# Kernel tuning notes

Hardware: AMD Instinct MI355X
Metric: run time of the kernel (lower is better)

Reference implementation:

```python
import jax, jax.numpy as jnp
import numpy as np

B, S, E = 256, 128, 1024


def setup_inputs() -> dict:
    key = jax.random.key(0)
    k1, k2, k3, k4, k5 = jax.random.split(key, 5)
    x = jax.random.normal(k1, (B, S, E), dtype=jnp.float32)
    # ragged bags: start in [0,32), length in [1,96] so end <= 128 and bags are non-empty
    starts = jax.random.randint(k2, (B,), 0, 32)
    lengths = jax.random.randint(k3, (B,), 1, 97)
    document_index = jnp.stack([starts, starts + lengths], axis=-1).astype(jnp.int32)  # [B,2]
    scale = 1.0 / np.sqrt(E)
    W = jax.random.normal(k4, (E, E), dtype=jnp.float32) * scale  # relationMatrix.weight
    u = jax.random.normal(k5, (1, E), dtype=jnp.float32) * scale  # relationVector.weight
    return {"x": x, "W": W, "u": u, "document_index": document_index}


def reference(x, W, u, document_index):
    # scores_bs = relationVector(tanh(relationMatrix(x)))  (bias-free linears)
    h = jnp.tanh(jnp.einsum('bse,fe->bsf', x, W))          # [B,S,E]
    scores = jnp.einsum('bse,e->bs', h, u[0])              # [B,S]
    # ragged mask: position s belongs to doc b iff start <= s < end
    idx = jnp.arange(S)[None, :]                            # [1,S]
    mask = (idx >= document_index[:, :1]) & (idx < document_index[:, 1:])  # [B,S]
    attn = jax.nn.softmax(jnp.where(mask, scores, -jnp.inf), axis=-1)      # [B,S]
    attn = jnp.where(mask, attn, 0.0)
    out_concat = jnp.einsum('bs,bse->be', attn, x)          # [B,E]
    # keep_attention in the original is the last bag's softmax weights;
    # here returned padded to length S (zeros outside the bag)
    keep_attention = attn[-1]                               # [S]
    return out_concat, keep_attention
```

## Files before the change

### kernel.cpp

```cpp
#include <hip/hip_runtime.h>
#include <math.h>

#define Bb 256
#define Ss 128
#define Ee 1024
#define BK 64
#define APAD 72
#define NMAX 2048

typedef __bf16 bf16x8 __attribute__((ext_vector_type(8)));
typedef float f32x4 __attribute__((ext_vector_type(4)));

typedef __attribute__((address_space(3))) unsigned int lds_u32;
typedef __attribute__((address_space(1))) unsigned int glb_u32;

static __device__ __forceinline__ unsigned short f2bf(float f) {
    unsigned int u = __float_as_uint(f);
    u += 0x7FFFu + ((u >> 16) & 1u);
    return (unsigned short)(u >> 16);
}
static __device__ __forceinline__ float bf2f(unsigned short h) {
    return __uint_as_float((unsigned int)h << 16);
}

__global__ void conv_all(const float* __restrict__ x,
                         const float* __restrict__ W,
                         const int* __restrict__ doc,
                         unsigned short* __restrict__ xb,
                         unsigned short* __restrict__ Wb,
                         int* __restrict__ list) {
    const int st = blockIdx.x, by = blockIdx.y, tid = threadIdx.x;
    if (by == Bb + 128) {
        if (st != 0) return;
        __shared__ int sc[256];
        const int b = tid;
        const int start = doc[2 * b], end = doc[2 * b + 1];
        const int s0 = start >> 4;
        const int ns = ((end + 15) >> 4) - s0;
        sc[b] = ns;
        __syncthreads();
        for (int d = 1; d < 256; d <<= 1) {
            int v = sc[b];
            int add = (b >= d) ? sc[b - d] : 0;
            __syncthreads();
            sc[b] = v + add;
            __syncthreads();
        }
        const int total = sc[255];
        const int off = sc[b] - ns;
        for (int i = 0; i < ns; ++i)
            list[off + i] = b * Ss + ((s0 + i) << 4);
        for (int i = total + b; i < NMAX; i += 256)
            list[i] = -1;
        return;
    }
    if (by >= Bb) {
        int i = ((((by - Bb) << 3) | st) << 8) | tid;
        float4 v = reinterpret_cast<const float4*>(W)[i];
        ushort4 o;
        o.x = f2bf(v.x); o.y = f2bf(v.y); o.z = f2bf(v.z); o.w = f2bf(v.w);
        reinterpret_cast<ushort4*>(Wb)[i] = o;
        return;
    }
    const int b = by;
    const int start = doc[2 * b], end = doc[2 * b + 1];
    const int strip0 = start >> 4;
    const int ns = ((end + 15) >> 4) - strip0;
    if (st < strip0 || st >= strip0 + ns) return;
    const size_t base = ((size_t)b * Ss + (st << 4)) * Ee;
    #pragma unroll
    for (int r = 0; r < 16; ++r) {
        size_t idx = base + (size_t)r * Ee + (tid << 2);
        float4 v = *reinterpret_cast<const float4*>(x + idx);
        ushort4 o;
        o.x = f2bf(v.x); o.y = f2bf(v.y); o.z = f2bf(v.z); o.w = f2bf(v.w);
        *reinterpret_cast<ushort4*>(xb + idx) = o;
    }
}

__global__ void convW_kernel(const float* __restrict__ W, unsigned short* __restrict__ Wb) {
    int i = blockIdx.x * blockDim.x + threadIdx.x;
    float4 v = reinterpret_cast<const float4*>(W)[i];
    ushort4 o;
    o.x = f2bf(v.x); o.y = f2bf(v.y); o.z = f2bf(v.z); o.w = f2bf(v.w);
    reinterpret_cast<ushort4*>(Wb)[i] = o;
}

__launch_bounds__(256, 4)
__global__ void scores_gemm_xb(const unsigned short* __restrict__ xb,
                               const unsigned short* __restrict__ Wb,
                               const float* __restrict__ u,
                               const int* __restrict__ list,
                               float* __restrict__ part) {
    __shared__ __align__(16) unsigned short As[64 * BK];
    __shared__ __align__(16) unsigned short Bs[256 * BK];

    const int mb = blockIdx.x;
    const int fg = blockIdx.y;

    int e0 = list[mb << 2];
    if (e0 < 0) return;
    int e[4];
    bool val[4];
    e[0] = e0; val[0] = true;
    #pragma unroll
    for (int j = 1; j < 4; ++j) {
        int v = list[(mb << 2) | j];
        val[j] = v >= 0;
        e[j] = val[j] ? v : e0;
    }

    const int tid  = threadIdx.x;
    const int wave = tid >> 6;
    const int lane = tid & 63;
    const int quad = lane >> 4;
    const int l16  = lane & 15;

    const unsigned short* wbase = Wb + (size_t)(fg * 256) * Ee;

    f32x4 acc[4][4];
    #pragma unroll
    for (int i = 0; i < 4; ++i)
        #pragma unroll
        for (int j = 0; j < 4; ++j) acc[i][j] = (f32x4){0.f, 0.f, 0.f, 0.f};

    for (int t = 0; t < 16; ++t) {
        const int k0 = t << 6;
        #pragma unroll
        for (int r = 0; r < 2; ++r) {
            int chunk = (r << 8) | tid;
            int arow = chunk >> 3;
            int c8 = (chunk & 7) ^ (arow & 7);
            __builtin_amdgcn_global_load_lds(
                (const glb_u32*)(xb + ((size_t)e[arow >> 4] + (arow & 15)) * Ee + k0 + (c8 << 3)),
                (lds_u32*)&As[chunk << 3], 16, 0, 0);
        }
        #pragma unroll
        for (int r = 0; r < 8; ++r) {
            int chunk = (r << 8) | tid;
            int brow = chunk >> 3;
            int c8 = (chunk & 7) ^ (brow & 7);
            __builtin_amdgcn_global_load_lds(
                (const glb_u32*)(wbase + (size_t)brow * Ee + k0 + (c8 << 3)),
                (lds_u32*)&Bs[chunk << 3], 16, 0, 0);
        }
        __syncthreads();

        #pragma unroll
        for (int kk = 0; kk < BK; kk += 32) {
            const int c8k = (kk >> 3) + quad;
            bf16x8 bf[4];
            #pragma unroll
            for (int j = 0; j < 4; ++j) {
                const int n = wave * 64 + j * 16 + l16;
                bf[j] = *reinterpret_cast<const bf16x8*>(
                    &Bs[((n << 3) | (c8k ^ (n & 7))) << 3]);
            }
            #pragma unroll
            for (int st = 0; st < 4; ++st) {
                const int ar = st * 16 + l16;
                bf16x8 af = *reinterpret_cast<const bf16x8*>(
                    &As[((ar << 3) | (c8k ^ (ar & 7))) << 3]);
                #pragma unroll
                for (int j = 0; j < 4; ++j)
                    acc[st][j] = __builtin_amdgcn_mfma_f32_16x16x32_bf16(af, bf[j], acc[st][j], 0, 0, 0);
            }
        }
        __syncthreads();
    }

    float* s_red = reinterpret_cast<float*>(As);
    float uj[4];
    #pragma unroll
    for (int j = 0; j < 4; ++j)
        uj[j] = u[fg * 256 + wave * 64 + j * 16 + l16];
    #pragma unroll
    for (int st = 0; st < 4; ++st) {
        float p[4];
        #pragma unroll
        for (int r = 0; r < 4; ++r) {
            p[r] = tanhf(acc[st][0][r]) * uj[0] + tanhf(acc[st][1][r]) * uj[1]
                 + tanhf(acc[st][2][r]) * uj[2] + tanhf(acc[st][3][r]) * uj[3];
        }
        #pragma unroll
        for (int off = 8; off >= 1; off >>= 1)
            #pragma unroll
            for (int r = 0; r < 4; ++r)
                p[r] += __shfl_xor(p[r], off, 16);
        if (l16 == 0)
            #pragma unroll
            for (int r = 0; r < 4; ++r)
                s_red[wave * 64 + st * 16 + quad * 4 + r] = p[r];
    }
    __syncthreads();
    if (tid < 64) {
        const int strip = tid >> 4;
        if (val[strip]) {
            float v = s_red[tid] + s_red[64 + tid] + s_red[128 + tid] + s_red[192 + tid];
            part[(((size_t)e[strip] + (tid & 15)) << 2) | fg] = v;
        }
    }
}

__launch_bounds__(256)
__global__ void scores_gemm_fb(const float* __restrict__ x,
                               const unsigned short* __restrict__ Wb,
                               const float* __restrict__ u,
                               const int* __restrict__ doc,
                               float* __restrict__ part) {
    __shared__ __align__(16) unsigned short As[8 * 16 * APAD];
    __shared__ __align__(16) unsigned short Bs[128 * BK];
    __shared__ float s_red[4][128];

    const int b  = blockIdx.x;
    const int ft = blockIdx.y;
    const int start = doc[2 * b], end = doc[2 * b + 1];
    const int strip0 = start >> 4;
    const int ns = ((end + 15) >> 4) - strip0;
    const int row0 = strip0 << 4;

    const int tid  = threadIdx.x;
    const int wave = tid >> 6;
    const int lane = tid & 63;
    const int quad = lane >> 4;
    const int l16  = lane & 15;
    const int arow = tid >> 4;
    const int acol = (tid & 15) << 2;

    const float* xbase = x + ((size_t)b * Ss + row0) * Ee;
    const unsigned short* wbase = Wb + (size_t)ft * 128 * Ee;

    f32x4 acc[8][2];
    #pragma unroll
    for (int i = 0; i < 8; ++i)
        #pragma unroll
        for (int j = 0; j < 2; ++j) acc[i][j] = (f32x4){0.f, 0.f, 0.f, 0.f};

    for (int k0 = 0; k0 < Ee; k0 += BK) {
        #pragma unroll
        for (int r = 0; r < 8; ++r) if (r < ns) {
            int row = (r << 4) | arow;
            float4 v = *reinterpret_cast<const float4*>(xbase + (size_t)row * Ee + k0 + acol);
            ushort4 o; o.x = f2bf(v.x); o.y = f2bf(v.y); o.z = f2bf(v.z); o.w = f2bf(v.w);
            *reinterpret_cast<ushort4*>(&As[row * APAD + acol]) = o;
        }
        #pragma unroll
        for (int r = 0; r < 4; ++r) {
            int chunk = (r << 8) | tid;
            int brow = chunk >> 3;
            int c8 = (chunk & 7) ^ (brow & 7);
            __builtin_amdgcn_global_load_lds(
                (const glb_u32*)(wbase + (size_t)brow * Ee + k0 + (c8 << 3)),
                (lds_u32*)&Bs[chunk << 3], 16, 0, 0);
        }
        __syncthreads();
        #pragma unroll
        for (int kk = 0; kk < BK; kk += 32) {
            const int n0 = wave * 32 + l16;
            const int n1 = n0 + 16;
            const int c8k = (kk >> 3) + quad;
            bf16x8 bf0 = *reinterpret_cast<const bf16x8*>(
                &Bs[((n0 << 3) | (c8k ^ (n0 & 7))) << 3]);
            bf16x8 bf1 = *reinterpret_cast<const bf16x8*>(
                &Bs[((n1 << 3) | (c8k ^ (n1 & 7))) << 3]);
            #pragma unroll
            for (int st = 0; st < 8; ++st) {
                if (st < ns) {
                    bf16x8 af = *reinterpret_cast<const bf16x8*>(
                        &As[(st * 16 + l16) * APAD + kk + quad * 8]);
                    acc[st][0] = __builtin_amdgcn_mfma_f32_16x16x32_bf16(af, bf0, acc[st][0], 0, 0, 0);
                    acc[st][1] = __builtin_amdgcn_mfma_f32_16x16x32_bf16(af, bf1, acc[st][1], 0, 0, 0);
                }
            }
        }
        __syncthreads();
    }

    const float u0 = u[ft * 128 + wave * 32 + l16];
    const float u1 = u[ft * 128 + wave * 32 + 16 + l16];
    #pragma unroll
    for (int st = 0; st < 8; ++st) {
        if (st < ns) {
            float p[4];
            #pragma unroll
            for (int r = 0; r < 4; ++r)
                p[r] = tanhf(acc[st][0][r]) * u0 + tanhf(acc[st][1][r]) * u1;
            #pragma unroll
            for (int off = 8; off >= 1; off >>= 1)
                #pragma unroll
                for (int r = 0; r < 4; ++r)
                    p[r] += __shfl_xor(p[r], off, 16);
            if (l16 == 0)
                #pragma unroll
                for (int r = 0; r < 4; ++r)
                    s_red[wave][st * 16 + quad * 4 + r] = p[r];
        }
    }
    __syncthreads();
    if (tid < (ns << 4)) {
        float v = s_red[0][tid] + s_red[1][tid] + s_red[2][tid] + s_red[3][tid];
        part[((size_t)(b * Ss + row0 + tid) << 3) | ft] = v;
    }
}

__global__ void out_fused(const unsigned short* __restrict__ xb,
                          const float* __restrict__ x,
                          const float* __restrict__ part,
                          const int* __restrict__ doc,
                          float* __restrict__ out,
                          float* __restrict__ keep,
                          int np8) {
    const int h = blockIdx.x, b = blockIdx.y, t = threadIdx.x;
    const int start = doc[2 * b], end = doc[2 * b + 1];
    __shared__ float a_s[Ss];
    __shared__ float red[2];
    __shared__ float4 red4[4][64];

    bool m = false;
    float sc = -INFINITY;
    if (t < Ss) {
        m = (t >= start) && (t < end);
        if (m) {
            const float* pp = part + (size_t)(b * Ss + t) * (np8 ? 8 : 4);
            float4 p0 = *reinterpret_cast<const float4*>(pp);
            sc = (p0.x + p0.y) + (p0.z + p0.w);
            if (np8) {
                float4 p1 = *reinterpret_cast<const float4*>(pp + 4);
                sc += (p1.x + p1.y) + (p1.z + p1.w);
            }
        }
    }
    float v = sc;
    #pragma unroll
    for (int off = 32; off >= 1; off >>= 1)
        v = fmaxf(v, __shfl_xor(v, off, 64));
    if (t < Ss && (t & 63) == 0) red[t >> 6] = v;
    __syncthreads();
    const float mx = fmaxf(red[0], red[1]);
    __syncthreads();
    const float e = m ? __expf(sc - mx) : 0.f;
    v = e;
    #pragma unroll
    for (int off = 32; off >= 1; off >>= 1)
        v += __shfl_xor(v, off, 64);
    if (t < Ss && (t & 63) == 0) red[t >> 6] = v;
    __syncthreads();
    if (t < Ss) a_s[t] = e / (red[0] + red[1]);
    __syncthreads();
    if (h == 0 && b == Bb - 1 && t < Ss) keep[t] = a_s[t];

    const int ssub = t >> 6, tt = t & 63;
    float4 accv = {0.f, 0.f, 0.f, 0.f};
    if (xb) {
        const unsigned short* xr = xb + (size_t)b * Ss * Ee + h * 256 + (tt << 2);
        for (int s = start + ssub; s < end; s += 4) {
            float a = a_s[s];
            ushort4 q = *reinterpret_cast<const ushort4*>(xr + (size_t)s * Ee);
            accv.x += a * bf2f(q.x); accv.y += a * bf2f(q.y);
            accv.z += a * bf2f(q.z); accv.w += a * bf2f(q.w);
        }
    } else {
        const float* xr = x + (size_t)b * Ss * Ee + h * 256 + (tt << 2);
        for (int s = start + ssub; s < end; s += 4) {
            float a = a_s[s];
            float4 q = *reinterpret_cast<const float4*>(xr + (size_t)s * Ee);
            accv.x += a * q.x; accv.y += a * q.y;
            accv.z += a * q.z; accv.w += a * q.w;
        }
    }
    red4[ssub][tt] = accv;
    __syncthreads();
    if (t < 64) {
        float4 r0 = red4[0][t], r1 = red4[1][t], r2 = red4[2][t], r3 = red4[3][t];
        float4 s;
        s.x = (r0.x + r1.x) + (r2.x + r3.x);
        s.y = (r0.y + r1.y) + (r2.y + r3.y);
        s.z = (r0.z + r1.z) + (r2.z + r3.z);
        s.w = (r0.w + r1.w) + (r2.w + r3.w);
        reinterpret_cast<float4*>(out + (size_t)b * Ee + h * 256)[t] = s;
    }
}

extern "C" void kernel_launch(void* const* d_in, const int* in_sizes, int n_in,
                              void* d_out, int out_size, void* d_ws, size_t ws_size,
                              hipStream_t stream) {
    const float* x  = (const float*)d_in[0];
    const float* W  = (const float*)d_in[1];
    const float* u  = (const float*)d_in[2];
    const int* doc  = (const int*)d_in[3];
    float* out = (float*)d_out;

    const size_t szWb   = (size_t)Ee * Ee * 2;
    const size_t szXb   = (size_t)Bb * Ss * Ee * 2;
    const size_t szPart = (size_t)Bb * Ss * 8 * 4;
    const size_t szList = (size_t)NMAX * 4;

    unsigned short* Wb = (unsigned short*)d_ws;
    const bool big_ws = ws_size >= szWb + szXb + szPart + szList;

    if (big_ws) {
        unsigned short* xbuf = (unsigned short*)((char*)d_ws + szWb);
        float* part = (float*)((char*)d_ws + szWb + szXb);
        int* list = (int*)((char*)d_ws + szWb + szXb + szPart);
        conv_all<<<dim3(8, Bb + 129), 256, 0, stream>>>(x, W, doc, xbuf, Wb, list);
        scores_gemm_xb<<<dim3(NMAX / 4, 4), 256, 0, stream>>>(xbuf, Wb, u, list, part);
        out_fused<<<dim3(4, Bb), 256, 0, stream>>>(xbuf, x, part, doc, out, out + (size_t)Bb * Ee, 0);
    } else {
        float* part = (float*)((char*)d_ws + szWb);
        convW_kernel<<<1024, 256, 0, stream>>>(W, Wb);
        scores_gemm_fb<<<dim3(Bb, 8), 256, 0, stream>>>(x, Wb, u, doc, part);
        out_fused<<<dim3(4, Bb), 256, 0, stream>>>(nullptr, x, part, doc, out, out + (size_t)Bb * Ee, 1);
    }
}
```

Measured before the change: 245.6 us.

## Load W fragments directly from global and double-buffer A tiles in LDS

The scores GEMM on the xb path no longer stages the W tile through LDS. Each lane reads its bf16x8 W fragments straight from global memory into registers, and only the x tile is staged, now in two LDS buffers so the next k-slice loads while the current one computes. This cuts LDS footprint and the per-iteration W staging and barrier work. In exchange, W reads are uncoalesced per-lane global loads that depend on cache hits, and the occupancy hint drops from 4 to 3 waves.

```diff
diff --git a/kernel.cpp b/kernel.cpp
--- a/kernel.cpp
+++ b/kernel.cpp
@@ -86,14 +86,14 @@
     reinterpret_cast<ushort4*>(Wb)[i] = o;
 }
 
-__launch_bounds__(256, 4)
+__launch_bounds__(256, 3)
 __global__ void scores_gemm_xb(const unsigned short* __restrict__ xb,
                                const unsigned short* __restrict__ Wb,
                                const float* __restrict__ u,
                                const int* __restrict__ list,
                                float* __restrict__ part) {
-    __shared__ __align__(16) unsigned short As[64 * BK];
-    __shared__ __align__(16) unsigned short Bs[256 * BK];
+    __shared__ __align__(16) unsigned short As[2][64 * BK];
+    __shared__ float s_red[4][64];
 
     const int mb = blockIdx.x;
     const int fg = blockIdx.y;
@@ -116,7 +116,7 @@
     const int quad = lane >> 4;
     const int l16  = lane & 15;
 
-    const unsigned short* wbase = Wb + (size_t)(fg * 256) * Ee;
+    const unsigned short* wrow = Wb + (size_t)(fg * 256 + wave * 64 + l16) * Ee + quad * 8;
 
     f32x4 acc[4][4];
     #pragma unroll
@@ -124,8 +124,7 @@
         #pragma unroll
         for (int j = 0; j < 4; ++j) acc[i][j] = (f32x4){0.f, 0.f, 0.f, 0.f};
 
-    for (int t = 0; t < 16; ++t) {
-        const int k0 = t << 6;
+    auto stageA = [&](int buf, int k0) {
         #pragma unroll
         for (int r = 0; r < 2; ++r) {
             int chunk = (r << 8) | tid;
@@ -133,34 +132,30 @@
             int c8 = (chunk & 7) ^ (arow & 7);
             __builtin_amdgcn_global_load_lds(
                 (const glb_u32*)(xb + ((size_t)e[arow >> 4] + (arow & 15)) * Ee + k0 + (c8 << 3)),
-                (lds_u32*)&As[chunk << 3], 16, 0, 0);
-        }
-        #pragma unroll
-        for (int r = 0; r < 8; ++r) {
-            int chunk = (r << 8) | tid;
-            int brow = chunk >> 3;
-            int c8 = (chunk & 7) ^ (brow & 7);
-            __builtin_amdgcn_global_load_lds(
-                (const glb_u32*)(wbase + (size_t)brow * Ee + k0 + (c8 << 3)),
-                (lds_u32*)&Bs[chunk << 3], 16, 0, 0);
-        }
-        __syncthreads();
+                (lds_u32*)&As[buf][chunk << 3], 16, 0, 0);
+        }
+    };
+
+    stageA(0, 0);
+    __syncthreads();
+
+    for (int t = 0; t < 16; ++t) {
+        const int k0 = t << 6;
+        const int cb = t & 1, nb = cb ^ 1;
+        if (t < 15) stageA(nb, k0 + 64);
 
         #pragma unroll
         for (int kk = 0; kk < BK; kk += 32) {
+            bf16x8 bf[4];
+            #pragma unroll
+            for (int j = 0; j < 4; ++j)
+                bf[j] = *reinterpret_cast<const bf16x8*>(wrow + (size_t)(j * 16) * Ee + k0 + kk);
             const int c8k = (kk >> 3) + quad;
-            bf16x8 bf[4];
-            #pragma unroll
-            for (int j = 0; j < 4; ++j) {
-                const int n = wave * 64 + j * 16 + l16;
-                bf[j] = *reinterpret_cast<const bf16x8*>(
-                    &Bs[((n << 3) | (c8k ^ (n & 7))) << 3]);
-            }
             #pragma unroll
             for (int st = 0; st < 4; ++st) {
                 const int ar = st * 16 + l16;
                 bf16x8 af = *reinterpret_cast<const bf16x8*>(
-                    &As[((ar << 3) | (c8k ^ (ar & 7))) << 3]);
+                    &As[cb][((ar << 3) | (c8k ^ (ar & 7))) << 3]);
                 #pragma unroll
                 for (int j = 0; j < 4; ++j)
                     acc[st][j] = __builtin_amdgcn_mfma_f32_16x16x32_bf16(af, bf[j], acc[st][j], 0, 0, 0);
@@ -169,7 +164,6 @@
         __syncthreads();
     }
 
-    float* s_red = reinterpret_cast<float*>(As);
     float uj[4];
     #pragma unroll
     for (int j = 0; j < 4; ++j)
@@ -190,13 +184,13 @@
         if (l16 == 0)
             #pragma unroll
             for (int r = 0; r < 4; ++r)
-                s_red[wave * 64 + st * 16 + quad * 4 + r] = p[r];
+                s_red[wave][st * 16 + quad * 4 + r] = p[r];
     }
     __syncthreads();
     if (tid < 64) {
         const int strip = tid >> 4;
         if (val[strip]) {
-            float v = s_red[tid] + s_red[64 + tid] + s_red[128 + tid] + s_red[192 + tid];
+            float v = s_red[0][tid] + s_red[1][tid] + s_red[2][tid] + s_red[3][tid];
             part[(((size_t)e[strip] + (tid & 15)) << 2) | fg] = v;
         }
     }
```

After: 277.5 us. 13.0% more time.
